# Kernel optimization log

Measured on AMD Instinct MI355X. Metric: run time of the kernel, lower is better.

## Reference

```python
import jax, jax.numpy as jnp
import numpy as np

N_EMBD = 1024
N_HEAD = 16
HEAD_DIM = N_EMBD // N_HEAD
B, S = 4, 1024


def setup_inputs() -> dict:
    key = jax.random.key(0)
    k1, k2, k3 = jax.random.split(key, 3)
    scale = 0.02
    return {
        "x": jax.random.normal(k1, (B, S, N_EMBD), dtype=jnp.float32),
        "Wqkv": jax.random.normal(k2, (N_EMBD, 3 * N_EMBD), dtype=jnp.float32) * scale,
        "bqkv": jnp.zeros((3 * N_EMBD,), dtype=jnp.float32),
        "Wproj": jax.random.normal(k3, (N_EMBD, N_EMBD), dtype=jnp.float32) * scale,
        "bproj": jnp.zeros((N_EMBD,), dtype=jnp.float32),
    }


def reference(x, Wqkv, bqkv, Wproj, bproj):
    b, s, e = x.shape
    qkv = x @ Wqkv + bqkv  # (b, s, 3e)
    q, k, v = jnp.split(qkv, 3, axis=-1)
    # (b, h, s, d)
    q = q.reshape(b, s, N_HEAD, HEAD_DIM).transpose(0, 2, 1, 3)
    k = k.reshape(b, s, N_HEAD, HEAD_DIM).transpose(0, 2, 1, 3)
    v = v.reshape(b, s, N_HEAD, HEAD_DIM).transpose(0, 2, 1, 3)
    scores = jnp.einsum("bhqd,bhkd->bhqk", q, k) / jnp.sqrt(
        jnp.asarray(HEAD_DIM, dtype=x.dtype)
    )
    causal = jnp.tril(jnp.ones((s, s), dtype=bool))  # (s, s)
    scores = jnp.where(causal[None, None, :, :], scores, jnp.asarray(-jnp.inf, dtype=scores.dtype))
    attn = jax.nn.softmax(scores, axis=-1)
    out = jnp.einsum("bhqk,bhkd->bhqd", attn, v)
    out = out.transpose(0, 2, 1, 3).reshape(b, s, e)
    return out @ Wproj + bproj
```

## Files before the change

### kernel.cpp

```cpp
#include <hip/hip_runtime.h>

#define S_LEN 1024
#define EMB   1024
#define NH    16
#define HD    64
#define BATCH 4
#define M_TOT 4096
#define QSZ   (BATCH * NH * S_LEN * HD)

typedef __attribute__((ext_vector_type(4))) float  f32x4;
typedef __attribute__((ext_vector_type(8))) __bf16 bf16x8;

__device__ __forceinline__ unsigned short f2bf(float f) {
  union { float f; unsigned u; } a; a.f = f;
  unsigned r = a.u + 0x7fffu + ((a.u >> 16) & 1u);
  return (unsigned short)(r >> 16);
}

__device__ __forceinline__ float fexp2(float x) {
#if __has_builtin(__builtin_amdgcn_exp2f)
  return __builtin_amdgcn_exp2f(x);
#else
  return exp2f(x);
#endif
}

__global__ void cvt_bf16(const float4* __restrict__ in, ushort4* __restrict__ out, int n4) {
  int i = blockIdx.x * blockDim.x + threadIdx.x;
  if (i >= n4) return;
  float4 v = in[i];
  ushort4 o;
  o.x = f2bf(v.x); o.y = f2bf(v.y); o.z = f2bf(v.z); o.w = f2bf(v.w);
  out[i] = o;
}

__global__ void cvt_transpose(const float* __restrict__ in, unsigned short* __restrict__ out,
                              int K, int N) {
  __shared__ unsigned short tile[32][33];
  int n0 = blockIdx.x * 32, k0 = blockIdx.y * 32;
  int tx = threadIdx.x, ty = threadIdx.y;
  #pragma unroll
  for (int r = ty; r < 32; r += 8)
    tile[r][tx] = f2bf(in[(size_t)(k0 + r) * N + n0 + tx]);
  __syncthreads();
  #pragma unroll
  for (int r = ty; r < 32; r += 8)
    out[(size_t)(n0 + r) * K + k0 + tx] = tile[tx][r];
}

__global__ __launch_bounds__(512, 2) void gemm_qkv256(
    const unsigned short* __restrict__ A,
    const unsigned short* __restrict__ Bt,
    const float* __restrict__ bias,
    unsigned short* __restrict__ O)
{
  __shared__ alignas(16) char smem[131072];
  const int m0 = blockIdx.x * 256, n0 = blockIdx.y * 256;
  const int K = EMB;
  const int t = threadIdx.x;
  const int wid = t >> 6, lane = t & 63;
  const int wm = wid >> 2, wn = wid & 3;
  const int lr = lane & 15, lg = lane >> 4;
  const int nkt = K >> 6;

  f32x4 acc[8][4] = {};

  auto STAGE = [&](int b, int kt) {
    const int k0 = kt << 6;
    #pragma unroll
    for (int l = 0; l < 4; ++l) {
      const int L = l * 8192 + t * 16;
      const int row = L >> 7;
      const int c = (L >> 4) & 7;
      const int ce = ((c ^ (row & 7)) << 3);
      const unsigned short* gA = A  + (size_t)(m0 + row) * K + k0 + ce;
      const unsigned short* gB = Bt + (size_t)(n0 + row) * K + k0 + ce;
      __builtin_amdgcn_global_load_lds(
          (const __attribute__((address_space(1))) unsigned int*)gA,
          (__attribute__((address_space(3))) unsigned int*)(smem + b * 32768 + L),
          16, 0, 0);
      __builtin_amdgcn_global_load_lds(
          (const __attribute__((address_space(1))) unsigned int*)gB,
          (__attribute__((address_space(3))) unsigned int*)(smem + 65536 + b * 32768 + L),
          16, 0, 0);
    }
  };

  STAGE(0, 0);

  for (int kt = 0; kt < nkt; ++kt) {
    const int cur = kt & 1;
    if (kt + 1 < nkt) {
      STAGE(cur ^ 1, kt + 1);
      asm volatile("s_waitcnt vmcnt(8)" ::: "memory");
    } else {
      asm volatile("s_waitcnt vmcnt(0)" ::: "memory");
    }
    __builtin_amdgcn_s_barrier();
    asm volatile("" ::: "memory");

    const char* Ab = smem + cur * 32768;
    const char* Bb = smem + 65536 + cur * 32768;
    #pragma unroll
    for (int s = 0; s < 2; ++s) {
      bf16x8 af[8], bfr[4];
      #pragma unroll
      for (int i = 0; i < 8; ++i) {
        const int row = wm * 128 + i * 16 + lr;
        const int byt = row * 128 + (((s * 4 + lg) ^ (row & 7)) << 4);
        af[i] = *(const bf16x8*)(Ab + byt);
      }
      #pragma unroll
      for (int j = 0; j < 4; ++j) {
        const int row = wn * 64 + j * 16 + lr;
        const int byt = row * 128 + (((s * 4 + lg) ^ (row & 7)) << 4);
        bfr[j] = *(const bf16x8*)(Bb + byt);
      }
      __builtin_amdgcn_s_setprio(1);
      #pragma unroll
      for (int i = 0; i < 8; ++i)
        #pragma unroll
        for (int j = 0; j < 4; ++j)
          acc[i][j] = __builtin_amdgcn_mfma_f32_16x16x32_bf16(af[i], bfr[j], acc[i][j], 0, 0, 0);
      __builtin_amdgcn_s_setprio(0);
    }
    asm volatile("s_waitcnt lgkmcnt(0)" ::: "memory");
    __builtin_amdgcn_s_barrier();
  }

  const int sec = n0 >> 10;
  if (sec < 2) {
    #pragma unroll
    for (int i = 0; i < 8; ++i)
      #pragma unroll
      for (int j = 0; j < 4; ++j) {
        const int col = n0 + wn * 64 + j * 16 + lr;
        const float bv = bias[col];
        const int cc = col & 1023, h = cc >> 6, d = cc & 63;
        #pragma unroll
        for (int r = 0; r < 4; ++r) {
          const int row = m0 + wm * 128 + i * 16 + lg * 4 + r;
          float v = acc[i][j][r] + bv;
          if (sec == 0) v *= 0.18033688f;
          const int bb = row >> 10, ss = row & 1023;
          O[(size_t)sec * QSZ + (((size_t)(bb * NH + h) * S_LEN + ss) * HD + d)] = f2bf(v);
        }
      }
  } else {
    unsigned short* T = (unsigned short*)smem;
    const int bb2 = m0 >> 10, sbase = m0 & 1023;
    #pragma unroll
    for (int qr = 0; qr < 2; ++qr)
      #pragma unroll
      for (int qc = 0; qc < 2; ++qc) {
        __syncthreads();
        if (wm == qr && (wn >> 1) == qc) {
          #pragma unroll
          for (int i = 0; i < 8; ++i)
            #pragma unroll
            for (int j = 0; j < 4; ++j) {
              const int ci = (wn & 1) * 64 + j * 16 + lr;
              const float bv = bias[n0 + qc * 128 + ci];
              union { ushort4 s4; __bf16 b[4]; } pk;
              #pragma unroll
              for (int r = 0; r < 4; ++r) pk.b[r] = (__bf16)(acc[i][j][r] + bv);
              *(ushort4*)(T + ci * 136 + i * 16 + lg * 4) = pk.s4;
            }
        }
        __syncthreads();
        const int ci = t >> 2, part = t & 3;
        const int cc = (n0 - 2048) + qc * 128 + ci;
        const int h = cc >> 6, d = cc & 63;
        unsigned short* dst = O + 2ull * QSZ +
            ((size_t)(bb2 * NH + h) * HD + d) * S_LEN + sbase + qr * 128;
        #pragma unroll
        for (int u = 0; u < 4; ++u) {
          const int spos = part * 32 + u * 8;
          *(bf16x8*)(dst + spos) = *(const bf16x8*)(T + ci * 136 + spos);
        }
      }
  }
}

__global__ __launch_bounds__(256) void gemm_proj(
    const unsigned short* __restrict__ A,
    const unsigned short* __restrict__ Bt,
    const float* __restrict__ bias,
    float* __restrict__ outp,
    int M, int N, int K)
{
  __shared__ alignas(16) char smem[49152];
  unsigned short* As = (unsigned short*)smem;
  unsigned short* Bs = (unsigned short*)(smem + 24576);
  const int m0 = blockIdx.x * 128, n0 = blockIdx.y * 128;
  const int t = threadIdx.x;
  const int wid = t >> 6, lane = t & 63;
  const int wr = wid >> 1, wc = wid & 1;
  const int lr = lane & 15, lg = lane >> 4;
  const int nkt = K >> 5;

  f32x4 acc[4][4] = {};

  auto STAGE = [&](int b, int kt) {
    const int k0 = kt << 5;
    #pragma unroll
    for (int c = 0; c < 2; ++c) {
      int idx8 = (c * 4 + wid) * 64 + lane;
      int row  = idx8 >> 2, col = (idx8 & 3) << 3;
      const unsigned short* gA = A  + (size_t)(m0 + row) * K + k0 + col;
      const unsigned short* gB = Bt + (size_t)(n0 + row) * K + k0 + col;
      __builtin_amdgcn_global_load_lds(
          (const __attribute__((address_space(1))) unsigned int*)gA,
          (__attribute__((address_space(3))) unsigned int*)(As + b * 4096 + (c * 4 + wid) * 512),
          16, 0, 0);
      __builtin_amdgcn_global_load_lds(
          (const __attribute__((address_space(1))) unsigned int*)gB,
          (__attribute__((address_space(3))) unsigned int*)(Bs + b * 4096 + (c * 4 + wid) * 512),
          16, 0, 0);
    }
  };

  STAGE(0, 0);
  STAGE(1, 1);

  for (int kt = 0; kt < nkt; ++kt) {
    if (kt + 2 < nkt) {
      STAGE((kt + 2) % 3, kt + 2);
      asm volatile("s_waitcnt vmcnt(8)" ::: "memory");
    } else if (kt + 1 < nkt) {
      asm volatile("s_waitcnt vmcnt(4)" ::: "memory");
    } else {
      asm volatile("s_waitcnt vmcnt(0)" ::: "memory");
    }
    __builtin_amdgcn_s_barrier();
    asm volatile("" ::: "memory");

    const unsigned short* Ab = As + (kt % 3) * 4096;
    const unsigned short* Bb = Bs + (kt % 3) * 4096;
    bf16x8 af[4], bfr[4];
    #pragma unroll
    for (int i = 0; i < 4; ++i)
      af[i] = *(const bf16x8*)(Ab + (wr * 64 + i * 16 + lr) * 32 + lg * 8);
    #pragma unroll
    for (int j = 0; j < 4; ++j)
      bfr[j] = *(const bf16x8*)(Bb + (wc * 64 + j * 16 + lr) * 32 + lg * 8);
    __builtin_amdgcn_s_setprio(1);
    #pragma unroll
    for (int i = 0; i < 4; ++i)
      #pragma unroll
      for (int j = 0; j < 4; ++j)
        acc[i][j] = __builtin_amdgcn_mfma_f32_16x16x32_bf16(af[i], bfr[j], acc[i][j], 0, 0, 0);
    __builtin_amdgcn_s_setprio(0);

    asm volatile("s_waitcnt lgkmcnt(0)" ::: "memory");
    __builtin_amdgcn_s_barrier();
  }

  #pragma unroll
  for (int i = 0; i < 4; ++i)
    #pragma unroll
    for (int j = 0; j < 4; ++j) {
      const int col = n0 + wc * 64 + j * 16 + lr;
      const float bv = bias[col];
      #pragma unroll
      for (int r = 0; r < 4; ++r) {
        const int row = m0 + wr * 64 + i * 16 + lg * 4 + r;
        outp[(size_t)row * (size_t)N + col] = acc[i][j][r] + bv;
      }
    }
}

__device__ __forceinline__ void group_tile(
    const bf16x8 (&kf)[8], const bf16x8 (&vf)[8], const bf16x8 (&qf)[2],
    int kt, int q0, bool diag, int lr, int lg,
    float& m, float& lp, f32x4 (&o)[4])
{
  f32x4 sacc[4] = {};
  __builtin_amdgcn_s_setprio(1);
  #pragma unroll
  for (int nt = 0; nt < 4; ++nt)
    #pragma unroll
    for (int kk = 0; kk < 2; ++kk)
      sacc[nt] = __builtin_amdgcn_mfma_f32_16x16x32_bf16(kf[nt * 2 + kk], qf[kk], sacc[nt], 0, 0, 0);
  __builtin_amdgcn_s_setprio(0);

  float p[16];
  if (diag) {
    const int q = q0 + lr;
    #pragma unroll
    for (int nt = 0; nt < 4; ++nt)
      #pragma unroll
      for (int r = 0; r < 4; ++r) {
        int k = kt * 64 + nt * 16 + lg * 4 + r;
        p[nt * 4 + r] = (k > q) ? -1e30f : sacc[nt][r];
      }
  } else {
    #pragma unroll
    for (int nt = 0; nt < 4; ++nt)
      #pragma unroll
      for (int r = 0; r < 4; ++r)
        p[nt * 4 + r] = sacc[nt][r];
  }

  float r8[8], r4[4];
  #pragma unroll
  for (int i = 0; i < 8; ++i) r8[i] = fmaxf(p[i], p[i + 8]);
  #pragma unroll
  for (int i = 0; i < 4; ++i) r4[i] = fmaxf(r8[i], r8[i + 4]);
  float pm = fmaxf(fmaxf(r4[0], r4[1]), fmaxf(r4[2], r4[3]));
  if (__any(pm > m + 11.5f)) {
    float px = fmaxf(pm, __shfl_xor(pm, 16, 64));
    px = fmaxf(px, __shfl_xor(px, 32, 64));
    float mn = fmaxf(m, px);
    float fs = fexp2(m - mn);
    lp *= fs;
    #pragma unroll
    for (int dt = 0; dt < 4; ++dt)
      #pragma unroll
      for (int r = 0; r < 4; ++r) o[dt][r] *= fs;
    m = mn;
  }
  #pragma unroll
  for (int i = 0; i < 16; ++i) p[i] = fexp2(p[i] - m);

  float s8[8], s4[4];
  #pragma unroll
  for (int i = 0; i < 8; ++i) s8[i] = p[i] + p[i + 8];
  #pragma unroll
  for (int i = 0; i < 4; ++i) s4[i] = s8[i] + s8[i + 4];
  lp += (s4[0] + s4[1]) + (s4[2] + s4[3]);

  union { unsigned u[8]; __bf16 b[16]; } W;
  #pragma unroll
  for (int i = 0; i < 16; ++i) W.b[i] = (__bf16)p[i];

  const int dl0 = ((2 * (lg & 1) + (lg >> 1)) * 16 + lr) << 2;
  const int dl1 = ((2 * ((lg & 1) ^ 1) + (lg >> 1)) * 16 + lr) << 2;
  const bool oddlg = (lg & 1) != 0;
  const bool hb    = (lg >> 1) != 0;
  union { unsigned u[4]; bf16x8 v; } T0, T1;
  #pragma unroll
  for (int kk = 0; kk < 2; ++kk) {
    #pragma unroll
    for (int c = 0; c < 2; ++c) {
      unsigned vlo = W.u[4 * kk + c];
      unsigned vhi = W.u[4 * kk + 2 + c];
      unsigned s0 = oddlg ? vhi : vlo;
      unsigned s1 = oddlg ? vlo : vhi;
      unsigned r0 = (unsigned)__builtin_amdgcn_ds_permute(dl0, (int)s0);
      unsigned r1 = (unsigned)__builtin_amdgcn_ds_permute(dl1, (int)s1);
      unsigned* T = kk ? T1.u : T0.u;
      T[c]     = hb ? r1 : r0;
      T[2 + c] = hb ? r0 : r1;
    }
  }

  __builtin_amdgcn_s_setprio(1);
  #pragma unroll
  for (int dt = 0; dt < 4; ++dt) {
    o[dt] = __builtin_amdgcn_mfma_f32_16x16x32_bf16(vf[dt * 2 + 0], T0.v, o[dt], 0, 0, 0);
    o[dt] = __builtin_amdgcn_mfma_f32_16x16x32_bf16(vf[dt * 2 + 1], T1.v, o[dt], 0, 0, 0);
  }
  __builtin_amdgcn_s_setprio(0);
}

__device__ __forceinline__ void group_epilogue(
    const f32x4 (&o)[4], float lp, int q0, int lr, int lg,
    char* Ep, unsigned short* __restrict__ attout, int bb, int h)
{
  float l2 = lp + __shfl_xor(lp, 16, 64);
  float l4 = l2 + __shfl_xor(l2, 32, 64);
  float rl = 1.0f / l4;
  #pragma unroll
  for (int dt = 0; dt < 4; ++dt) {
    union { ushort4 s4; __bf16 b[4]; } ov;
    #pragma unroll
    for (int r = 0; r < 4; ++r) ov.b[r] = (__bf16)(o[dt][r] * rl);
    int byt = (lr * 128 + (dt * 16 + lg * 4) * 2) ^ ((lr & 7) << 4);
    *(ushort4*)(Ep + byt) = ov.s4;
  }
  asm volatile("s_waitcnt lgkmcnt(0)" ::: "memory");
  const int lane = lr + lg * 16;
  const int ql = lane >> 2, c = lane & 3;
  #pragma unroll
  for (int s = 0; s < 2; ++s) {
    int byt = (ql * 128 + (c * 16 + s * 8) * 2) ^ ((ql & 7) << 4);
    bf16x8 vrow = *(const bf16x8*)(Ep + byt);
    *(bf16x8*)(attout + (size_t)(bb * S_LEN + q0 + ql) * EMB + h * HD + c * 16 + s * 8) = vrow;
  }
}

__global__ __launch_bounds__(256, 2) void attn_fwd(
    const unsigned short* __restrict__ Q,
    const unsigned short* __restrict__ K,
    const unsigned short* __restrict__ Vt,
    unsigned short* __restrict__ attout)
{
  __shared__ alignas(16) char stage[2][16384];
  __shared__ alignas(16) char Ep_lds[4][2048];
  const int bid = blockIdx.x;
  const int bh   = ((bid & 7) << 3) | ((bid >> 3) & 7);
  const int base = bid >> 6;
  const int wv = threadIdx.x >> 6, lane = threadIdx.x & 63;
  const int pi = base * 4 + wv;
  const int lr = lane & 15, lg = lane >> 4;
  const int nkt  = 16 - base;
  const int nktl = base + 1;
  const int q0h = (63 - pi) * 16, q0l = pi * 16;
  const unsigned short* Qb = Q  + (size_t)bh * (S_LEN * HD);
  const unsigned short* Kh = K  + (size_t)bh * (S_LEN * HD);
  const unsigned short* Vh = Vt + (size_t)bh * (HD * S_LEN);
  const int bb = bh >> 4, h = bh & 15;

  auto STAGE = [&](int b, int kt) {
    char* lb = &stage[b][0];
    #pragma unroll
    for (int j = 0; j < 4; ++j) {
      if (wv < 2) {
        int L = wv * 4096 + j * 1024 + lane * 16;
        int row = L >> 7, c = (L >> 4) & 7;
        const unsigned short* src = Kh + (size_t)(kt * 64 + row) * HD + ((c ^ (row & 7)) << 3);
        __builtin_amdgcn_global_load_lds(
            (const __attribute__((address_space(1))) unsigned int*)src,
            (__attribute__((address_space(3))) unsigned int*)(lb + wv * 4096 + j * 1024),
            16, 0, 0);
      } else {
        int L = (wv - 2) * 4096 + j * 1024 + lane * 16;
        int row = L >> 7, c = (L >> 4) & 7;
        const unsigned short* src = Vh + (size_t)row * S_LEN + kt * 64 + ((c ^ (row & 7)) << 3);
        __builtin_amdgcn_global_load_lds(
            (const __attribute__((address_space(1))) unsigned int*)src,
            (__attribute__((address_space(3))) unsigned int*)(lb + 8192 + (wv - 2) * 4096 + j * 1024),
            16, 0, 0);
      }
    }
  };

  bf16x8 qfh[2], qfl[2];
  #pragma unroll
  for (int kk = 0; kk < 2; ++kk) {
    qfh[kk] = *(const bf16x8*)(Qb + (size_t)(q0h + lr) * HD + kk * 32 + lg * 8);
    qfl[kk] = *(const bf16x8*)(Qb + (size_t)(q0l + lr) * HD + kk * 32 + lg * 8);
  }

  float mh = -1e30f, lph = 0.f, ml = -1e30f, lpl = 0.f;
  f32x4 oh[4] = {}, ol[4] = {};

  STAGE(0, 0);
  asm volatile("s_waitcnt vmcnt(0)" ::: "memory");
  __syncthreads();

  for (int kt = 0; kt < nkt; ++kt) {
    const int cur = kt & 1;
    if (kt + 1 < nkt) STAGE(cur ^ 1, kt + 1);

    const char* sb = &stage[cur][0];
    bf16x8 kf[8], vf[8];
    #pragma unroll
    for (int nt = 0; nt < 4; ++nt)
      #pragma unroll
      for (int kk = 0; kk < 2; ++kk) {
        const int byt = (nt * 16 + lr) * 128 + ((((kk << 2) + lg) ^ (lr & 7)) << 4);
        kf[nt * 2 + kk] = *(const bf16x8*)(sb + byt);
        vf[nt * 2 + kk] = *(const bf16x8*)(sb + 8192 + byt);
      }

    group_tile(kf, vf, qfh, kt, q0h, kt == nkt - 1, lr, lg, mh, lph, oh);
    if (kt < nktl)
      group_tile(kf, vf, qfl, kt, q0l, kt == nktl - 1, lr, lg, ml, lpl, ol);

    asm volatile("s_waitcnt vmcnt(0)" ::: "memory");
    __syncthreads();
  }

  char* Ep = &Ep_lds[wv][0];
  group_epilogue(oh, lph, q0h, lr, lg, Ep, attout, bb, h);
  group_epilogue(ol, lpl, q0l, lr, lg, Ep, attout, bb, h);
}

extern "C" void kernel_launch(void* const* d_in, const int* in_sizes, int n_in,
                              void* d_out, int out_size, void* d_ws, size_t ws_size,
                              hipStream_t stream) {
  const float* x     = (const float*)d_in[0];
  const float* Wqkv  = (const float*)d_in[1];
  const float* bqkv  = (const float*)d_in[2];
  const float* Wproj = (const float*)d_in[3];
  const float* bproj = (const float*)d_in[4];

  unsigned short* xb     = (unsigned short*)d_ws;
  unsigned short* WqkvT  = xb     + (size_t)M_TOT * EMB;
  unsigned short* WprojT = WqkvT  + (size_t)3 * EMB * EMB;
  unsigned short* qkv    = WprojT + (size_t)EMB * EMB;
  unsigned short* att    = qkv    + 3ull * QSZ;

  cvt_bf16<<<dim3((M_TOT * EMB / 4 + 255) / 256), dim3(256), 0, stream>>>(
      (const float4*)x, (ushort4*)xb, M_TOT * EMB / 4);
  cvt_transpose<<<dim3(3 * EMB / 32, EMB / 32), dim3(32, 8), 0, stream>>>(Wqkv, WqkvT, EMB, 3 * EMB);
  cvt_transpose<<<dim3(EMB / 32, EMB / 32), dim3(32, 8), 0, stream>>>(Wproj, WprojT, EMB, EMB);

  gemm_qkv256<<<dim3(M_TOT / 256, 3 * EMB / 256), dim3(512), 0, stream>>>(
      xb, WqkvT, bqkv, qkv);

  attn_fwd<<<dim3(8 * BATCH * NH), dim3(256), 0, stream>>>(
      qkv, qkv + QSZ, qkv + 2ull * QSZ, att);

  gemm_proj<<<dim3(M_TOT / 128, EMB / 128), dim3(256), 0, stream>>>(
      att, WprojT, bproj, (float*)d_out, M_TOT, EMB, EMB);
}
```

Before: 98.67 us.

## Restructure QKV GEMM mainloop into 8-phase ping-pong schedule with half-tile prefetch

Replaces the simple double-buffered K loop of the QKV projection GEMM with a hand-scheduled 8-phase pipeline. Each phase reads quarter-fragments of A/B from LDS, issues one half-tile global-to-LDS load for a future K tile, and runs a quarter block of MFMAs between barriers, in the style of HipKittens. The intent is to interleave LDS reads, global loads and MFMA work more finely so memory latency is hidden behind matrix math. In exchange it adds many more barriers per K step and relies on intricate vmcnt accounting, which risks stalls or races.

```diff
diff --git a/kernel.cpp b/kernel.cpp
--- a/kernel.cpp
+++ b/kernel.cpp
@@ -56,76 +56,106 @@
 {
   __shared__ alignas(16) char smem[131072];
   const int m0 = blockIdx.x * 256, n0 = blockIdx.y * 256;
-  const int K = EMB;
   const int t = threadIdx.x;
   const int wid = t >> 6, lane = t & 63;
   const int wm = wid >> 2, wn = wid & 3;
   const int lr = lane & 15, lg = lane >> 4;
-  const int nkt = K >> 6;
 
   f32x4 acc[8][4] = {};
-
-  auto STAGE = [&](int b, int kt) {
-    const int k0 = kt << 6;
-    #pragma unroll
-    for (int l = 0; l < 4; ++l) {
+  bf16x8 af[4][2], bfA[2][2], bfB[2][2];
+
+  auto SH = [&](int buf, int mat, int half, int tile) {
+    const int k0 = tile << 6;
+    const unsigned short* base = mat ? Bt : A;
+    const int rbase = (mat ? n0 : m0) + half * 128;
+    char* dst = smem + buf * 65536 + mat * 32768 + half * 16384;
+    #pragma unroll
+    for (int l = 0; l < 2; ++l) {
       const int L = l * 8192 + t * 16;
-      const int row = L >> 7;
-      const int c = (L >> 4) & 7;
-      const int ce = ((c ^ (row & 7)) << 3);
-      const unsigned short* gA = A  + (size_t)(m0 + row) * K + k0 + ce;
-      const unsigned short* gB = Bt + (size_t)(n0 + row) * K + k0 + ce;
+      const int row = L >> 7, c = (L >> 4) & 7;
+      const unsigned short* g = base + (size_t)(rbase + row) * EMB + k0 + ((c ^ (row & 7)) << 3);
       __builtin_amdgcn_global_load_lds(
-          (const __attribute__((address_space(1))) unsigned int*)gA,
-          (__attribute__((address_space(3))) unsigned int*)(smem + b * 32768 + L),
+          (const __attribute__((address_space(1))) unsigned int*)g,
+          (__attribute__((address_space(3))) unsigned int*)(dst + L),
           16, 0, 0);
-      __builtin_amdgcn_global_load_lds(
-          (const __attribute__((address_space(1))) unsigned int*)gB,
-          (__attribute__((address_space(3))) unsigned int*)(smem + 65536 + b * 32768 + L),
-          16, 0, 0);
-    }
-  };
-
-  STAGE(0, 0);
-
-  for (int kt = 0; kt < nkt; ++kt) {
-    const int cur = kt & 1;
-    if (kt + 1 < nkt) {
-      STAGE(cur ^ 1, kt + 1);
-      asm volatile("s_waitcnt vmcnt(8)" ::: "memory");
+    }
+  };
+  auto READ_A = [&](int buf, int qi) {
+    const char* Ab = smem + buf * 65536 + wm * 16384;
+    #pragma unroll
+    for (int i = 0; i < 4; ++i)
+      #pragma unroll
+      for (int kk = 0; kk < 2; ++kk) {
+        const int row = qi * 64 + i * 16 + lr;
+        af[i][kk] = *(const bf16x8*)(Ab + row * 128 + (((kk * 4 + lg) ^ (row & 7)) << 4));
+      }
+  };
+  auto READ_B = [&](int buf, int qj, bf16x8 (&bf)[2][2]) {
+    const char* Bb = smem + buf * 65536 + 32768 + (wn >> 1) * 16384;
+    #pragma unroll
+    for (int jj = 0; jj < 2; ++jj)
+      #pragma unroll
+      for (int kk = 0; kk < 2; ++kk) {
+        const int row = (wn & 1) * 64 + qj * 32 + jj * 16 + lr;
+        bf[jj][kk] = *(const bf16x8*)(Bb + row * 128 + (((kk * 4 + lg) ^ (row & 7)) << 4));
+      }
+  };
+  auto BAR = [&] {
+    asm volatile("" ::: "memory");
+    __builtin_amdgcn_s_barrier();
+    asm volatile("" ::: "memory");
+  };
+  auto MFMAQ = [&](bf16x8 (&bf)[2][2], int ib, int jb) {
+    __builtin_amdgcn_s_setprio(1);
+    #pragma unroll
+    for (int i = 0; i < 4; ++i)
+      #pragma unroll
+      for (int jj = 0; jj < 2; ++jj)
+        #pragma unroll
+        for (int kk = 0; kk < 2; ++kk)
+          acc[ib + i][jb + jj] = __builtin_amdgcn_mfma_f32_16x16x32_bf16(
+              af[i][kk], bf[jj][kk], acc[ib + i][jb + jj], 0, 0, 0);
+    __builtin_amdgcn_s_setprio(0);
+  };
+
+  SH(0, 1, 0, 0); SH(0, 0, 0, 0); SH(0, 1, 1, 0); SH(0, 0, 1, 0);
+  SH(1, 1, 0, 1); SH(1, 0, 0, 1);
+  asm volatile("s_waitcnt vmcnt(4)" ::: "memory");
+  BAR();
+
+  for (int j = 0; j < 8; ++j) {
+    const bool nl = (j < 7);
+    const int t1 = 2 * j + 1, t2 = 2 * j + 2, t3 = 2 * j + 3;
+    READ_A(0, 0); READ_B(0, 0, bfA);
+    SH(1, 1, 1, t1);
+    BAR(); MFMAQ(bfA, 0, 0); BAR();
+    READ_B(0, 1, bfB);
+    SH(1, 0, 1, t1);
+    BAR(); MFMAQ(bfB, 0, 2); BAR();
+    READ_A(0, 1);
+    if (nl) SH(0, 1, 0, t2);
+    BAR(); MFMAQ(bfB, 4, 2); BAR();
+    if (nl) {
+      SH(0, 0, 0, t2);
+      asm volatile("s_waitcnt vmcnt(4)" ::: "memory");
     } else {
       asm volatile("s_waitcnt vmcnt(0)" ::: "memory");
     }
-    __builtin_amdgcn_s_barrier();
-    asm volatile("" ::: "memory");
-
-    const char* Ab = smem + cur * 32768;
-    const char* Bb = smem + 65536 + cur * 32768;
-    #pragma unroll
-    for (int s = 0; s < 2; ++s) {
-      bf16x8 af[8], bfr[4];
-      #pragma unroll
-      for (int i = 0; i < 8; ++i) {
-        const int row = wm * 128 + i * 16 + lr;
-        const int byt = row * 128 + (((s * 4 + lg) ^ (row & 7)) << 4);
-        af[i] = *(const bf16x8*)(Ab + byt);
-      }
-      #pragma unroll
-      for (int j = 0; j < 4; ++j) {
-        const int row = wn * 64 + j * 16 + lr;
-        const int byt = row * 128 + (((s * 4 + lg) ^ (row & 7)) << 4);
-        bfr[j] = *(const bf16x8*)(Bb + byt);
-      }
-      __builtin_amdgcn_s_setprio(1);
-      #pragma unroll
-      for (int i = 0; i < 8; ++i)
-        #pragma unroll
-        for (int j = 0; j < 4; ++j)
-          acc[i][j] = __builtin_amdgcn_mfma_f32_16x16x32_bf16(af[i], bfr[j], acc[i][j], 0, 0, 0);
-      __builtin_amdgcn_s_setprio(0);
-    }
-    asm volatile("s_waitcnt lgkmcnt(0)" ::: "memory");
-    __builtin_amdgcn_s_barrier();
+    BAR(); MFMAQ(bfA, 4, 0); BAR();
+    READ_A(1, 0); READ_B(1, 0, bfA);
+    if (nl) SH(0, 1, 1, t2);
+    BAR(); MFMAQ(bfA, 0, 0); BAR();
+    READ_B(1, 1, bfB);
+    if (nl) SH(0, 0, 1, t2);
+    BAR(); MFMAQ(bfB, 0, 2); BAR();
+    READ_A(1, 1);
+    if (nl) SH(1, 1, 0, t3);
+    BAR(); MFMAQ(bfB, 4, 2); BAR();
+    if (nl) {
+      SH(1, 0, 0, t3);
+      asm volatile("s_waitcnt vmcnt(4)" ::: "memory");
+    }
+    BAR(); MFMAQ(bfA, 4, 0); BAR();
   }
 
   const int sec = n0 >> 10;
```

Result: faster. 95.32 us (-3.4%).
